# Performance work log

Hardware: AMD Instinct MI355X
Metric: run time of the kernel (lower is better)

The kernel has to match this reference:

```python
import jax, jax.numpy as jnp
import numpy as np

N_NODES = 81920
N_EDGES = 1310720
NODES_PER_GRAPH = 320
N_GRAPHS = N_NODES // NODES_PER_GRAPH  # 256
IN_DIM = 64
HID = 64
OUT = 64


def setup_inputs() -> dict:
    key = jax.random.key(0)
    ks = jax.random.split(key, 16)
    x = jax.random.normal(ks[0], (N_NODES, IN_DIM), dtype=jnp.float32)
    edge_index = jax.random.randint(ks[1], (2, N_EDGES), 0, N_NODES, dtype=jnp.int32)
    # sorted graph-membership vector: 256 graphs of 320 nodes each
    batch = (jnp.arange(N_NODES, dtype=jnp.int32) // NODES_PER_GRAPH)
    std = 1.0  # module re-inits nn.Linear weights with N(0, 1)
    dims = [(IN_DIM, HID), (HID, HID), (HID, OUT)]
    params = {}
    for i, (di, do) in enumerate(dims):
        params[f"Wl{i}"] = std * jax.random.normal(ks[2 + 3 * i], (di, do), dtype=jnp.float32)
        params[f"bl{i}"] = jnp.zeros((do,), dtype=jnp.float32)
        params[f"Wr{i}"] = std * jax.random.normal(ks[3 + 3 * i], (di, do), dtype=jnp.float32)
    return dict(x=x, edge_index=edge_index, batch=batch, **params)


def _sage_conv(x, src, dst, Wl, bl, Wr):
    # PyG SAGEConv (aggr='mean', root_weight=True):
    #   out = lin_l(mean_{j in N(i)} x_j) + lin_r(x_i)
    msg = x[src]                                              # [E, d] gather
    agg = jax.ops.segment_sum(msg, dst, num_segments=N_NODES)  # [N, d] scatter-add
    cnt = jax.ops.segment_sum(jnp.ones((src.shape[0],), x.dtype), dst,
                              num_segments=N_NODES)
    agg = agg / jnp.maximum(cnt, 1.0)[:, None]                # mean aggregation
    return agg @ Wl + bl + x @ Wr


def reference(x, edge_index, batch, Wl0, bl0, Wr0, Wl1, bl1, Wr1, Wl2, bl2, Wr2):
    src, dst = edge_index[0], edge_index[1]
    layers = [(Wl0, bl0, Wr0), (Wl1, bl1, Wr1), (Wl2, bl2, Wr2)]
    h = x
    for i, (Wl, bl, Wr) in enumerate(layers):
        h = _sage_conv(h, src, dst, Wl, bl, Wr)
        if i < len(layers) - 1:
            h = jax.nn.relu(h)
            # F.dropout is identity in eval mode (training=False)
    # unbatch + take node 0 of every graph: first index where batch == g
    first_idx = jnp.searchsorted(batch, jnp.arange(N_GRAPHS, dtype=batch.dtype))
    return h[first_idx]  # [N_GRAPHS, OUT]
```

## Files before the change

kernel.cpp:

```cpp
#include <hip/hip_runtime.h>

#define N_NODES 81920
#define N_EDGES 1310720
#define NG 256
#define D 64
#define TM 64
#define SA 65
#define SB 33
#define NB 320
#define NBLK 1280
#define BMW 2560
#define HCHUNK 4096
#define EPT 16
#define CAP0 1280
#define CAP1 256
#define CAP2 64

typedef __attribute__((ext_vector_type(2))) short sbf2;

__device__ __forceinline__ bool tb(const unsigned* bm, int i) {
    return (bm[i >> 5] >> (i & 31)) & 1u;
}
__device__ __forceinline__ unsigned bf16rne(float f) {
    unsigned u = __float_as_uint(f);
    return (u + 0x7fffu + ((u >> 16) & 1u)) >> 16;
}


__global__ __launch_bounds__(256) void init_ws(float4* __restrict__ aggb4,
                                               unsigned* __restrict__ bms,
                                               int* __restrict__ indeg,
                                               int* __restrict__ n01,
                                               int* __restrict__ cur0,
                                               int* __restrict__ cur1,
                                               int* __restrict__ cur2) {
    int t = blockIdx.x * 256 + threadIdx.x;
    float4 z = make_float4(0.f, 0.f, 0.f, 0.f);
    aggb4[t] = z;
    aggb4[t + NBLK * 256] = z;
    if (t < 3 * BMW) bms[t] = 0u;
    if (t < N_NODES) indeg[t] = 0;
    if (t < 2) n01[t] = 0;
    if (t < NBLK) {
        cur0[t] = t * CAP0;
        cur1[t] = t * CAP1;
        cur2[t] = t * CAP2;
    }
}


__global__ void ff_mark(const int* __restrict__ batch, int* __restrict__ fidx,
                        unsigned* __restrict__ bm2, unsigned* __restrict__ bm1,
                        float* __restrict__ aggf) {
    int i = blockIdx.x * 256 + threadIdx.x;
    int b = batch[i];
    if (i == 0 || batch[i - 1] != b) {
        fidx[b] = i;
        unsigned bit = 1u << (i & 31);
        atomicOr(&bm2[i >> 5], bit);
        atomicOr(&bm1[i >> 5], bit);
        float4* r = (float4*)&aggf[i * D];
        #pragma unroll
        for (int j = 0; j < 16; ++j) r[j] = make_float4(0.f, 0.f, 0.f, 0.f);
    }
}

__global__ void mark_srcs_bm(const int* __restrict__ src, const int* __restrict__ dst,
                             const unsigned* __restrict__ bmD, unsigned* __restrict__ bmS,
                             const unsigned* __restrict__ orsrc) {
    if (orsrc && blockIdx.x == 0) {
        for (int w = threadIdx.x; w < BMW; w += 256)
            if (orsrc[w]) atomicOr(&bmS[w], orsrc[w]);
    }
    int e = blockIdx.x * 256 + threadIdx.x;
    if (e < N_EDGES && tb(bmD, dst[e])) {
        int s = src[e];
        atomicOr(&bmS[s >> 5], 1u << (s & 31));
    }
}


__global__ __launch_bounds__(256) void build(const int* __restrict__ src,
                                             const int* __restrict__ dst,
                                             const unsigned* __restrict__ bm0,
                                             const unsigned* __restrict__ bm1,
                                             const unsigned* __restrict__ bm2,
                                             int* __restrict__ cur0,
                                             int* __restrict__ cur1,
                                             int* __restrict__ cur2,
                                             int* __restrict__ esp0,
                                             int* __restrict__ esp1,
                                             int* __restrict__ esp2,
                                             int* __restrict__ indeg,
                                             int* __restrict__ list1,
                                             int* __restrict__ n1) {
    __shared__ int h0[NBLK];
    __shared__ int b0[NBLK];
    const int tid = threadIdx.x;
    const int e0  = blockIdx.x * HCHUNK;

    for (int i = tid; i < NBLK; i += 256) h0[i] = 0;

    {
        int i = blockIdx.x * 256 + tid;
        int lane = tid & 63;
        bool p1 = tb(bm1, i);
        unsigned long long b1 = __ballot(p1);
        int lt = __popcll(b1 & ((1ull << lane) - 1));
        int base = 0;
        if (lane == 0 && b1) base = atomicAdd(n1, __popcll(b1));
        base = __shfl(base, 0);
        if (p1) list1[base + lt] = i;
    }
    __syncthreads();

    int pk_r[EPT];
    int sb_r[EPT];
    int rk_r[EPT];

    #pragma unroll
    for (int j = 0; j < EPT; ++j) {
        int e = e0 + j * 256 + tid;
        int d = dst[e];
        sb_r[j] = -1;
        if (tb(bm0, d)) {
            int s  = src[e];
            int sb = s >> 6;
            int pk = (d << 6) | (s & 63);
            pk_r[j] = pk;
            sb_r[j] = sb;
            rk_r[j] = atomicAdd(&h0[sb], 1);
            atomicAdd(&indeg[d], 1);
            if (tb(bm1, d)) {
                int p1 = atomicAdd(&cur1[sb], 1);
                if (p1 < sb * CAP1 + CAP1) esp1[p1] = pk;
                if (tb(bm2, d)) {
                    int p2 = atomicAdd(&cur2[sb], 1);
                    if (p2 < sb * CAP2 + CAP2) esp2[p2] = pk;
                }
            }
        }
    }
    __syncthreads();

    for (int i = tid; i < NBLK; i += 256) {
        int c = h0[i];
        b0[i] = c ? atomicAdd(&cur0[i], c) : 0;
    }
    __syncthreads();

    #pragma unroll
    for (int j = 0; j < EPT; ++j) {
        int sb = sb_r[j];
        if (sb >= 0) {
            int pos = b0[sb] + rk_r[j];
            if (pos < sb * CAP0 + CAP0) esp0[pos] = pk_r[j];
        }
    }
}


__global__ __launch_bounds__(256, 8) void sage_push_bf(
    const float* __restrict__ hin, const int* __restrict__ cur,
    const int* __restrict__ esp, unsigned* __restrict__ aggb, int cap)
{
    __shared__ unsigned Rs[TM * SB];

    const int tid  = threadIdx.x;
    const int base = blockIdx.x * TM;
    const int lane = tid & 63;
    const int w    = tid >> 6;
    const int l5   = lane & 31;
    const int hi   = lane >> 5;

    const int e0 = blockIdx.x * cap;
    const int e1 = min(cur[blockIdx.x], e0 + cap);
    if (e0 == e1) return;

    for (int idx = tid; idx < TM * 32; idx += 256) {
        int m = idx >> 5, k = idx & 31;
        float2 v = *(const float2*)&hin[((base + m) << 6) + (k << 1)];
        Rs[m * SB + k] = bf16rne(v.x) | (bf16rne(v.y) << 16);
    }
    __syncthreads();

    const int chunk = ((e1 - e0) + 3) >> 2;
    int e = e0 + w * chunk;
    const int ee = min(e + chunk, e1);

    for (; e + 64 <= ee; e += 64) {
        int pv = esp[e + lane];
        #pragma unroll
        for (int u = 0; u < 32; ++u) {
            int p = __shfl(pv, (u << 1) + hi);
            unsigned v = Rs[(p & 63) * SB + l5];
            __builtin_amdgcn_global_atomic_fadd_v2bf16(
                (sbf2*)&aggb[((p >> 6) << 5) + l5], *(sbf2*)&v);
        }
    }
    for (; e < ee; ++e) {
        int p = esp[e];
        if (!hi) {
            unsigned v = Rs[(p & 63) * SB + l5];
            __builtin_amdgcn_global_atomic_fadd_v2bf16(
                (sbf2*)&aggb[((p >> 6) << 5) + l5], *(sbf2*)&v);
        }
    }
}


__global__ __launch_bounds__(256, 8) void sage_push_f32(
    const float* __restrict__ hin, const int* __restrict__ cur,
    const int* __restrict__ esp, float* __restrict__ agg, int cap)
{
    __shared__ float Rs[TM * SA];

    const int tid  = threadIdx.x;
    const int base = blockIdx.x * TM;
    const int lane = tid & 63;
    const int w    = tid >> 6;

    const int e0 = blockIdx.x * cap;
    const int e1 = min(cur[blockIdx.x], e0 + cap);
    if (e0 == e1) return;

    for (int idx = tid; idx < TM * D; idx += 256) {
        int m = idx >> 6, k = idx & 63;
        Rs[m * SA + k] = hin[(base << 6) + idx];
    }
    __syncthreads();

    const int chunk = ((e1 - e0) + 3) >> 2;
    int e = e0 + w * chunk;
    const int ee = min(e + chunk, e1);

    for (; e < ee; ++e) {
        int p = esp[e];
        atomicAdd(&agg[(p & 0x7fffffc0) + lane], Rs[(p & 63) * SA + lane]);
    }
}


__global__ __launch_bounds__(256, 4) void sage_finish_dense(
    const float* __restrict__ hin, unsigned* __restrict__ aggb,
    const int* __restrict__ indeg, float* __restrict__ hout,
    const float* __restrict__ Wl, const float* __restrict__ bl,
    const float* __restrict__ Wr)
{
    __shared__ float As[TM * SA];
    __shared__ float Xs[TM * SA];
    __shared__ float invs[TM];

    const int tid  = threadIdx.x;
    const int base = blockIdx.x * TM;

    if (tid < TM) invs[tid] = 1.0f / (float)max(indeg[base + tid], 1);
    for (int idx = tid; idx < TM * 32; idx += 256) {
        int m = idx >> 5, k2 = idx & 31;
        unsigned v = aggb[(base << 5) + idx];
        As[m * SA + (k2 << 1)]     = __uint_as_float(v << 16);
        As[m * SA + (k2 << 1) + 1] = __uint_as_float(v & 0xffff0000u);
        aggb[(base << 5) + idx] = 0u;
    }
    for (int idx = tid; idx < TM * D; idx += 256) {
        int m = idx >> 6, k = idx & 63;
        Xs[m * SA + k] = hin[(base << 6) + idx];
    }
    __syncthreads();
    for (int idx = tid; idx < TM * D; idx += 256) {
        int m = idx >> 6, k = idx & 63;
        As[m * SA + k] *= invs[m];
    }
    __syncthreads();

    const int j0 = (tid & 15) << 2;
    const int m0 = (tid >> 4) << 2;
    float o[4][4];
    float4 b4 = *(const float4*)&bl[j0];
    #pragma unroll
    for (int mi = 0; mi < 4; ++mi) {
        o[mi][0] = b4.x; o[mi][1] = b4.y; o[mi][2] = b4.z; o[mi][3] = b4.w;
    }
    #pragma unroll 8
    for (int k = 0; k < D; ++k) {
        float4 wl = *(const float4*)&Wl[(k << 6) + j0];
        float4 wr = *(const float4*)&Wr[(k << 6) + j0];
        #pragma unroll
        for (int mi = 0; mi < 4; ++mi) {
            float a = As[(m0 + mi) * SA + k];
            float x = Xs[(m0 + mi) * SA + k];
            o[mi][0] += a * wl.x + x * wr.x;
            o[mi][1] += a * wl.y + x * wr.y;
            o[mi][2] += a * wl.z + x * wr.z;
            o[mi][3] += a * wl.w + x * wr.w;
        }
    }
    #pragma unroll
    for (int mi = 0; mi < 4; ++mi) {
        float4 r = make_float4(fmaxf(o[mi][0], 0.f), fmaxf(o[mi][1], 0.f),
                               fmaxf(o[mi][2], 0.f), fmaxf(o[mi][3], 0.f));
        *(float4*)&hout[(base + m0 + mi) * D + j0] = r;
    }
}


__global__ __launch_bounds__(256, 4) void sage_finish_sel(
    const float* __restrict__ hin, unsigned* __restrict__ aggb,
    const int* __restrict__ indeg, const int* __restrict__ list,
    const int* __restrict__ pcount, float* __restrict__ hout,
    const float* __restrict__ Wl, const float* __restrict__ bl,
    const float* __restrict__ Wr)
{
    __shared__ float As[TM * SA];
    __shared__ float Xs[TM * SA];
    __shared__ float invs[TM];
    __shared__ int   nid[TM];

    const int cntv = *pcount;
    const int base = blockIdx.x * TM;
    if (base >= cntv) return;

    const int tid = threadIdx.x;
    if (tid < TM) {
        int n = (base + tid < cntv) ? list[base + tid] : -1;
        nid[tid]  = n;
        invs[tid] = (n >= 0) ? 1.0f / (float)max(indeg[n], 1) : 0.f;
    }
    __syncthreads();
    for (int idx = tid; idx < TM * 32; idx += 256) {
        int m = idx >> 5, k2 = idx & 31;
        int n = nid[m];
        if (n >= 0) {
            unsigned v = aggb[(n << 5) + k2];
            As[m * SA + (k2 << 1)]     = __uint_as_float(v << 16) * invs[m];
            As[m * SA + (k2 << 1) + 1] = __uint_as_float(v & 0xffff0000u) * invs[m];
        } else {
            As[m * SA + (k2 << 1)]     = 0.f;
            As[m * SA + (k2 << 1) + 1] = 0.f;
        }
    }
    for (int idx = tid; idx < TM * D; idx += 256) {
        int m = idx >> 6, k = idx & 63;
        int n = nid[m];
        Xs[m * SA + k] = (n >= 0) ? hin[n * D + k] : 0.f;
    }
    __syncthreads();

    const int j0 = (tid & 15) << 2;
    const int m0 = (tid >> 4) << 2;
    float o[4][4];
    float4 b4 = *(const float4*)&bl[j0];
    #pragma unroll
    for (int mi = 0; mi < 4; ++mi) {
        o[mi][0] = b4.x; o[mi][1] = b4.y; o[mi][2] = b4.z; o[mi][3] = b4.w;
    }
    #pragma unroll 8
    for (int k = 0; k < D; ++k) {
        float4 wl = *(const float4*)&Wl[(k << 6) + j0];
        float4 wr = *(const float4*)&Wr[(k << 6) + j0];
        #pragma unroll
        for (int mi = 0; mi < 4; ++mi) {
            float a = As[(m0 + mi) * SA + k];
            float x = Xs[(m0 + mi) * SA + k];
            o[mi][0] += a * wl.x + x * wr.x;
            o[mi][1] += a * wl.y + x * wr.y;
            o[mi][2] += a * wl.z + x * wr.z;
            o[mi][3] += a * wl.w + x * wr.w;
        }
    }
    #pragma unroll
    for (int mi = 0; mi < 4; ++mi) {
        int n = nid[m0 + mi];
        if (n >= 0) {
            float4 r = make_float4(fmaxf(o[mi][0], 0.f), fmaxf(o[mi][1], 0.f),
                                   fmaxf(o[mi][2], 0.f), fmaxf(o[mi][3], 0.f));
            *(float4*)&hout[n * D + j0] = r;
        }
    }
}


__global__ __launch_bounds__(256, 3) void final_gemm_sel(
    const float* __restrict__ hin, const float* __restrict__ agg,
    const int* __restrict__ indeg, const int* __restrict__ fidx,
    const float* __restrict__ Wl, const float* __restrict__ bl,
    const float* __restrict__ Wr, float* __restrict__ out)
{
    __shared__ float As[TM * SA];
    __shared__ float Xs[TM * SA];
    __shared__ int   nid[TM];
    __shared__ float invs[TM];

    const int tid  = threadIdx.x;
    const int base = blockIdx.x * TM;

    if (tid < TM) {
        int n = fidx[base + tid];
        nid[tid]  = n;
        invs[tid] = 1.0f / (float)max(indeg[n], 1);
    }
    __syncthreads();
    for (int idx = tid; idx < TM * D; idx += 256) {
        int m = idx >> 6, k = idx & 63;
        int n = nid[m];
        As[m * SA + k] = agg[n * D + k] * invs[m];
        Xs[m * SA + k] = hin[n * D + k];
    }
    __syncthreads();

    const int j0 = (tid & 15) << 2;
    const int m0 = (tid >> 4) << 2;
    float o[4][4];
    float4 b4 = *(const float4*)&bl[j0];
    #pragma unroll
    for (int mi = 0; mi < 4; ++mi) {
        o[mi][0] = b4.x; o[mi][1] = b4.y; o[mi][2] = b4.z; o[mi][3] = b4.w;
    }
    #pragma unroll 8
    for (int k = 0; k < D; ++k) {
        float4 wl = *(const float4*)&Wl[(k << 6) + j0];
        float4 wr = *(const float4*)&Wr[(k << 6) + j0];
        #pragma unroll
        for (int mi = 0; mi < 4; ++mi) {
            float a = As[(m0 + mi) * SA + k];
            float x = Xs[(m0 + mi) * SA + k];
            o[mi][0] += a * wl.x + x * wr.x;
            o[mi][1] += a * wl.y + x * wr.y;
            o[mi][2] += a * wl.z + x * wr.z;
            o[mi][3] += a * wl.w + x * wr.w;
        }
    }
    #pragma unroll
    for (int mi = 0; mi < 4; ++mi) {
        float4 r = make_float4(o[mi][0], o[mi][1], o[mi][2], o[mi][3]);
        *(float4*)&out[(base + m0 + mi) * D + j0] = r;
    }
}


extern "C" void kernel_launch(void* const* d_in, const int* in_sizes, int n_in,
                              void* d_out, int out_size, void* d_ws, size_t ws_size,
                              hipStream_t stream)
{
    const float* x     = (const float*)d_in[0];
    const int*   ei    = (const int*)d_in[1];
    const int*   batch = (const int*)d_in[2];
    const float* Wl0 = (const float*)d_in[3];
    const float* bl0 = (const float*)d_in[4];
    const float* Wr0 = (const float*)d_in[5];
    const float* Wl1 = (const float*)d_in[6];
    const float* bl1 = (const float*)d_in[7];
    const float* Wr1 = (const float*)d_in[8];
    const float* Wl2 = (const float*)d_in[9];
    const float* bl2 = (const float*)d_in[10];
    const float* Wr2 = (const float*)d_in[11];
    float* out = (float*)d_out;

    const int* src = ei;
    const int* dst = ei + N_EDGES;

    char* ws = (char*)d_ws;
    size_t off = 0;
    auto alloc = [&](size_t bytes) -> void* {
        void* p = ws + off;
        off = (off + bytes + 255) & ~(size_t)255;
        return p;
    };
    int*      cur0  = (int*)alloc(NBLK * sizeof(int));
    int*      cur1  = (int*)alloc(NBLK * sizeof(int));
    int*      cur2  = (int*)alloc(NBLK * sizeof(int));
    int*      fidx  = (int*)alloc(NG * sizeof(int));
    int*      list1 = (int*)alloc(N_NODES * sizeof(int));
    int*      esp0  = (int*)alloc((size_t)NBLK * CAP0 * sizeof(int));
    int*      esp1  = (int*)alloc((size_t)NBLK * CAP1 * sizeof(int));
    int*      esp2  = (int*)alloc((size_t)NBLK * CAP2 * sizeof(int));
    unsigned* aggb  = (unsigned*)alloc((size_t)N_NODES * 32 * sizeof(unsigned));
    float*    aggf  = (float*)alloc((size_t)N_NODES * D * sizeof(float));
    float*    h1    = (float*)alloc((size_t)N_NODES * D * sizeof(float));
    float*    h2    = (float*)alloc((size_t)N_NODES * D * sizeof(float));
    unsigned* bms   = (unsigned*)alloc((size_t)3 * BMW * sizeof(unsigned));
    int*      indeg = (int*)alloc(N_NODES * sizeof(int));
    int*      n01   = (int*)alloc(64 * sizeof(int));
    unsigned* bm0 = bms;
    unsigned* bm1 = bms + BMW;
    unsigned* bm2 = bms + 2 * BMW;
    int* n1 = n01 + 1;
    (void)ws_size; (void)in_sizes; (void)n_in; (void)out_size;

    const int EB = (N_EDGES + 255) / 256;

    init_ws<<<NBLK, 256, 0, stream>>>((float4*)aggb, bms, indeg, n01, cur0, cur1, cur2);
    ff_mark<<<NB, 256, 0, stream>>>(batch, fidx, bm2, bm1, aggf);
    mark_srcs_bm<<<EB, 256, 0, stream>>>(src, dst, bm2, bm1, (const unsigned*)nullptr);
    mark_srcs_bm<<<EB, 256, 0, stream>>>(src, dst, bm1, bm0, bm1);
    build<<<NB, 256, 0, stream>>>(src, dst, bm0, bm1, bm2, cur0, cur1, cur2,
                                  esp0, esp1, esp2, indeg, list1, n1);

    sage_push_bf     <<<NBLK, 256, 0, stream>>>(x, cur0, esp0, aggb, CAP0);
    sage_finish_dense<<<NBLK, 256, 0, stream>>>(x, aggb, indeg, h1, Wl0, bl0, Wr0);
    sage_push_bf     <<<NBLK, 256, 0, stream>>>(h1, cur1, esp1, aggb, CAP1);
    sage_finish_sel  <<<NBLK, 256, 0, stream>>>(h1, aggb, indeg, list1, n1,
                                                h2, Wl1, bl1, Wr1);
    sage_push_f32    <<<NBLK, 256, 0, stream>>>(h2, cur2, esp2, aggf, CAP2);
    final_gemm_sel   <<<NG / TM, 256, 0, stream>>>(h2, aggf, indeg, fidx, Wl2, bl2, Wr2, out);
}
```

Measured before the change: 404.4 us.

## Fuse layer-1 push into dense finish kernel and replace init kernel with memset

```diff
diff --git a/kernel.cpp b/kernel.cpp
--- a/kernel.cpp
+++ b/kernel.cpp
@@ -27,32 +27,15 @@
 }
 
 
-__global__ __launch_bounds__(256) void init_ws(float4* __restrict__ aggb4,
-                                               unsigned* __restrict__ bms,
-                                               int* __restrict__ indeg,
-                                               int* __restrict__ n01,
-                                               int* __restrict__ cur0,
-                                               int* __restrict__ cur1,
-                                               int* __restrict__ cur2) {
-    int t = blockIdx.x * 256 + threadIdx.x;
-    float4 z = make_float4(0.f, 0.f, 0.f, 0.f);
-    aggb4[t] = z;
-    aggb4[t + NBLK * 256] = z;
-    if (t < 3 * BMW) bms[t] = 0u;
-    if (t < N_NODES) indeg[t] = 0;
-    if (t < 2) n01[t] = 0;
-    if (t < NBLK) {
-        cur0[t] = t * CAP0;
-        cur1[t] = t * CAP1;
-        cur2[t] = t * CAP2;
-    }
-}
-
-
 __global__ void ff_mark(const int* __restrict__ batch, int* __restrict__ fidx,
                         unsigned* __restrict__ bm2, unsigned* __restrict__ bm1,
-                        float* __restrict__ aggf) {
+                        float* __restrict__ aggf,
+                        int* __restrict__ cur0, int* __restrict__ cur1,
+                        int* __restrict__ cur2) {
     int i = blockIdx.x * 256 + threadIdx.x;
+    if (i < NBLK) {
+        cur0[i] = i * CAP0; cur1[i] = i * CAP1; cur2[i] = i * CAP2;
+    }
     int b = batch[i];
     if (i == 0 || batch[i - 1] != b) {
         fidx[b] = i;
@@ -114,9 +97,7 @@
     }
     __syncthreads();
 
-    int pk_r[EPT];
-    int sb_r[EPT];
-    int rk_r[EPT];
+    int pk_r[EPT], sb_r[EPT], rk_r[EPT];
 
     #pragma unroll
     for (int j = 0; j < EPT; ++j) {
@@ -241,26 +222,28 @@
 }
 
 
-__global__ __launch_bounds__(256, 4) void sage_finish_dense(
-    const float* __restrict__ hin, unsigned* __restrict__ aggb,
+__global__ __launch_bounds__(256, 4) void finish_dense_push1(
+    const float* __restrict__ hin, const unsigned* __restrict__ aggbA,
     const int* __restrict__ indeg, float* __restrict__ hout,
     const float* __restrict__ Wl, const float* __restrict__ bl,
-    const float* __restrict__ Wr)
+    const float* __restrict__ Wr,
+    const int* __restrict__ cur1, const int* __restrict__ esp1,
+    unsigned* __restrict__ aggbB)
 {
     __shared__ float As[TM * SA];
     __shared__ float Xs[TM * SA];
     __shared__ float invs[TM];
 
     const int tid  = threadIdx.x;
-    const int base = blockIdx.x * TM;
+    const int t    = blockIdx.x;
+    const int base = t * TM;
 
     if (tid < TM) invs[tid] = 1.0f / (float)max(indeg[base + tid], 1);
     for (int idx = tid; idx < TM * 32; idx += 256) {
         int m = idx >> 5, k2 = idx & 31;
-        unsigned v = aggb[(base << 5) + idx];
+        unsigned v = aggbA[(base << 5) + idx];
         As[m * SA + (k2 << 1)]     = __uint_as_float(v << 16);
         As[m * SA + (k2 << 1) + 1] = __uint_as_float(v & 0xffff0000u);
-        aggb[(base << 5) + idx] = 0u;
     }
     for (int idx = tid; idx < TM * D; idx += 256) {
         int m = idx >> 6, k = idx & 63;
@@ -295,17 +278,59 @@
             o[mi][3] += a * wl.w + x * wr.w;
         }
     }
-    #pragma unroll
-    for (int mi = 0; mi < 4; ++mi) {
-        float4 r = make_float4(fmaxf(o[mi][0], 0.f), fmaxf(o[mi][1], 0.f),
-                               fmaxf(o[mi][2], 0.f), fmaxf(o[mi][3], 0.f));
-        *(float4*)&hout[(base + m0 + mi) * D + j0] = r;
+
+    float4 r[4];
+    #pragma unroll
+    for (int mi = 0; mi < 4; ++mi) {
+        r[mi] = make_float4(fmaxf(o[mi][0], 0.f), fmaxf(o[mi][1], 0.f),
+                            fmaxf(o[mi][2], 0.f), fmaxf(o[mi][3], 0.f));
+        *(float4*)&hout[(base + m0 + mi) * D + j0] = r[mi];
+    }
+
+    const int e0 = t * CAP1;
+    const int e1 = min(cur1[t], e0 + CAP1);
+    if (e0 == e1) return;
+
+    __syncthreads();
+    unsigned* Rs = (unsigned*)As;
+    #pragma unroll
+    for (int mi = 0; mi < 4; ++mi) {
+        Rs[(m0 + mi) * SB + (j0 >> 1)]     = bf16rne(r[mi].x) | (bf16rne(r[mi].y) << 16);
+        Rs[(m0 + mi) * SB + (j0 >> 1) + 1] = bf16rne(r[mi].z) | (bf16rne(r[mi].w) << 16);
+    }
+    __syncthreads();
+
+    const int lane = tid & 63;
+    const int w    = tid >> 6;
+    const int l5   = lane & 31;
+    const int hi   = lane >> 5;
+    const int chunk = ((e1 - e0) + 3) >> 2;
+    int e = e0 + w * chunk;
+    const int ee = min(e + chunk, e1);
+
+    for (; e + 64 <= ee; e += 64) {
+        int pv = esp1[e + lane];
+        #pragma unroll
+        for (int u = 0; u < 32; ++u) {
+            int p = __shfl(pv, (u << 1) + hi);
+            unsigned v = Rs[(p & 63) * SB + l5];
+            __builtin_amdgcn_global_atomic_fadd_v2bf16(
+                (sbf2*)&aggbB[((p >> 6) << 5) + l5], *(sbf2*)&v);
+        }
+    }
+    for (; e < ee; ++e) {
+        int p = esp1[e];
+        if (!hi) {
+            unsigned v = Rs[(p & 63) * SB + l5];
+            __builtin_amdgcn_global_atomic_fadd_v2bf16(
+                (sbf2*)&aggbB[((p >> 6) << 5) + l5], *(sbf2*)&v);
+        }
     }
 }
 
 
 __global__ __launch_bounds__(256, 4) void sage_finish_sel(
-    const float* __restrict__ hin, unsigned* __restrict__ aggb,
+    const float* __restrict__ hin, const unsigned* __restrict__ aggb,
     const int* __restrict__ indeg, const int* __restrict__ list,
     const int* __restrict__ pcount, float* __restrict__ hout,
     const float* __restrict__ Wl, const float* __restrict__ bl,
@@ -466,6 +491,13 @@
         off = (off + bytes + 255) & ~(size_t)255;
         return p;
     };
+    char* zb = ws;
+    unsigned* aggbA = (unsigned*)alloc((size_t)N_NODES * 32 * sizeof(unsigned));
+    unsigned* aggbB = (unsigned*)alloc((size_t)N_NODES * 32 * sizeof(unsigned));
+    unsigned* bms   = (unsigned*)alloc((size_t)3 * BMW * sizeof(unsigned));
+    int*      indeg = (int*)alloc(N_NODES * sizeof(int));
+    int*      n01   = (int*)alloc(64 * sizeof(int));
+    size_t zbytes = off;
     int*      cur0  = (int*)alloc(NBLK * sizeof(int));
     int*      cur1  = (int*)alloc(NBLK * sizeof(int));
     int*      cur2  = (int*)alloc(NBLK * sizeof(int));
@@ -474,13 +506,9 @@
     int*      esp0  = (int*)alloc((size_t)NBLK * CAP0 * sizeof(int));
     int*      esp1  = (int*)alloc((size_t)NBLK * CAP1 * sizeof(int));
     int*      esp2  = (int*)alloc((size_t)NBLK * CAP2 * sizeof(int));
-    unsigned* aggb  = (unsigned*)alloc((size_t)N_NODES * 32 * sizeof(unsigned));
     float*    aggf  = (float*)alloc((size_t)N_NODES * D * sizeof(float));
     float*    h1    = (float*)alloc((size_t)N_NODES * D * sizeof(float));
     float*    h2    = (float*)alloc((size_t)N_NODES * D * sizeof(float));
-    unsigned* bms   = (unsigned*)alloc((size_t)3 * BMW * sizeof(unsigned));
-    int*      indeg = (int*)alloc(N_NODES * sizeof(int));
-    int*      n01   = (int*)alloc(64 * sizeof(int));
     unsigned* bm0 = bms;
     unsigned* bm1 = bms + BMW;
     unsigned* bm2 = bms + 2 * BMW;
@@ -489,18 +517,19 @@
 
     const int EB = (N_EDGES + 255) / 256;
 
-    init_ws<<<NBLK, 256, 0, stream>>>((float4*)aggb, bms, indeg, n01, cur0, cur1, cur2);
-    ff_mark<<<NB, 256, 0, stream>>>(batch, fidx, bm2, bm1, aggf);
+    hipMemsetAsync(zb, 0, zbytes, stream);
+
+    ff_mark<<<NB, 256, 0, stream>>>(batch, fidx, bm2, bm1, aggf, cur0, cur1, cur2);
     mark_srcs_bm<<<EB, 256, 0, stream>>>(src, dst, bm2, bm1, (const unsigned*)nullptr);
     mark_srcs_bm<<<EB, 256, 0, stream>>>(src, dst, bm1, bm0, bm1);
     build<<<NB, 256, 0, stream>>>(src, dst, bm0, bm1, bm2, cur0, cur1, cur2,
                                   esp0, esp1, esp2, indeg, list1, n1);
 
-    sage_push_bf     <<<NBLK, 256, 0, stream>>>(x, cur0, esp0, aggb, CAP0);
-    sage_finish_dense<<<NBLK, 256, 0, stream>>>(x, aggb, indeg, h1, Wl0, bl0, Wr0);
-    sage_push_bf     <<<NBLK, 256, 0, stream>>>(h1, cur1, esp1, aggb, CAP1);
-    sage_finish_sel  <<<NBLK, 256, 0, stream>>>(h1, aggb, indeg, list1, n1,
-                                                h2, Wl1, bl1, Wr1);
-    sage_push_f32    <<<NBLK, 256, 0, stream>>>(h2, cur2, esp2, aggf, CAP2);
-    final_gemm_sel   <<<NG / TM, 256, 0, stream>>>(h2, aggf, indeg, fidx, Wl2, bl2, Wr2, out);
-}
+    sage_push_bf<<<NBLK, 256, 0, stream>>>(x, cur0, esp0, aggbA, CAP0);
+    finish_dense_push1<<<NBLK, 256, 0, stream>>>(x, aggbA, indeg, h1, Wl0, bl0, Wr0,
+                                                 cur1, esp1, aggbB);
+    sage_finish_sel<<<NBLK, 256, 0, stream>>>(h1, aggbB, indeg, list1, n1,
+                                              h2, Wl1, bl1, Wr1);
+    sage_push_f32<<<NBLK, 256, 0, stream>>>(h2, cur2, esp2, aggf, CAP2);
+    final_gemm_sel<<<NG / TM, 256, 0, stream>>>(h2, aggf, indeg, fidx, Wl2, bl2, Wr2, out);
+}
```

Measured after the change: 410.9 us. Within noise of the previous version (+1.6%).
